# Performance work log

Hardware: AMD Instinct MI355X
Metric: run time of the kernel (lower is better)

The kernel has to match this reference:

```python
import math
import jax, jax.numpy as jnp
import numpy as np


def setup_inputs() -> dict:
    key = jax.random.key(0)
    k1, k2 = jax.random.split(key)
    N, H, W, h, d = 32, 32, 32, 16, 64
    input_NHWhd = jax.random.normal(k1, (N, H, W, h, d), dtype=jnp.float32)
    emb_2dd = jax.random.uniform(k2, (2, d, d), dtype=jnp.float32) * (2.0 * math.pi)
    return {"input_NHWhd": input_NHWhd, "emb_2dd": emb_2dd}


def _positions(H, W):
    # xlim = sqrt(W/H), ylim = sqrt(H/W); positions stacked as (y, x)
    xlim = math.sqrt(W / H)
    ylim = math.sqrt(H / W)
    x_HW = jnp.broadcast_to(jnp.linspace(-xlim, xlim, W, dtype=jnp.float32)[None, :], (H, W))
    y_HW = jnp.broadcast_to(jnp.linspace(-ylim, ylim, H, dtype=jnp.float32)[:, None], (H, W))
    return jnp.stack((y_HW, x_HW), axis=-1)  # [H, W, 2]


def reference(input_NHWhd, emb_2dd):
    N, H, W, h, d = input_NHWhd.shape
    # skew-symmetric generator bases (the -0.5 shift cancels in M - M^T,
    # kept for faithfulness to the original)
    upper_2dd = jnp.triu(emb_2dd, k=1) - 0.5
    skew_2dd = upper_2dd - jnp.swapaxes(upper_2dd, -2, -1)  # [2, d, d]
    pos_HW2 = _positions(H, W)
    # per-position generator: sum over the 2 spatial components
    gen_HWdd = jnp.einsum("hwc,cij->hwij", pos_HW2, skew_2dd)  # [H, W, d, d]
    rot_HWdd = jax.vmap(jax.scipy.linalg.expm)(gen_HWdd.reshape(-1, d, d)).reshape(H, W, d, d)
    # apply rotation: out[n,y,x,q,:] = input[n,y,x,q,:] @ rot[y,x]
    out_NHWhd = jnp.einsum("nhwqd,hwde->nhwqe", input_NHWhd, rot_HWdd.astype(input_NHWhd.dtype))
    return out_NHWhd
```

## Files before the change

### kernel.cpp

```cpp
#include <hip/hip_runtime.h>


typedef float f4 __attribute__((ext_vector_type(4)));
typedef short s8v __attribute__((ext_vector_type(8)));
typedef float f32x4 __attribute__((ext_vector_type(4)));
typedef unsigned short ush;
typedef unsigned int u32;
typedef ush us4 __attribute__((ext_vector_type(4)));

constexpr int LST = 68;
constexpr int BST = 72;
constexpr int SLOT = 64 * BST;

static __device__ __forceinline__ ush f2bf(float f) {
    u32 u = __float_as_uint(f);
    u += 0x7fffu + ((u >> 16) & 1u);
    return (ush)(u >> 16);
}
static __device__ __forceinline__ float bf2f(ush h) {
    return __uint_as_float(((u32)h) << 16);
}
static __device__ __forceinline__ s8v negbf(s8v v) {
    u32* p = (u32*)&v;
#pragma unroll
    for (int i = 0; i < 4; ++i) p[i] ^= 0x80008000u;
    return v;
}
static __device__ __forceinline__ u32 cvtpk(float a, float b) {
    u32 r;
    asm("v_cvt_pk_bf16_f32 %0, %1, %2" : "=v"(r) : "v"(a), "v"(b));
    return r;
}

static __device__ __forceinline__ void load_frag(
    s8v fr[2][2][2], const ush* __restrict__ ah, const ush* __restrict__ al,
    int m, int q4, int base, bool neg)
{
#pragma unroll
    for (int t = 0; t < 2; ++t)
#pragma unroll
        for (int ks = 0; ks < 2; ++ks) {
            const int off = (base + t * 16 + m) * BST + ks * 32 + q4 * 8;
            s8v h = *(const s8v*)&ah[off];
            s8v l = *(const s8v*)&al[off];
            if (neg) { h = negbf(h); l = negbf(l); }
            fr[t][ks][0] = h;
            fr[t][ks][1] = l;
        }
}

static __device__ __forceinline__ void mm_pre(
    ush* __restrict__ dh, ush* __restrict__ dl,
    const s8v pa[2][2][2],
    const ush* __restrict__ qh, const ush* __restrict__ ql,
    float cdiag, int m, int q4, int DM, int DN)
{
    s8v qb[2][2][2];
    load_frag(qb, qh, ql, m, q4, DN, false);

    f32x4 acc[2][2];
#pragma unroll
    for (int mt = 0; mt < 2; ++mt)
#pragma unroll
        for (int nt = 0; nt < 2; ++nt) acc[mt][nt] = (f32x4){0.f, 0.f, 0.f, 0.f};

#pragma unroll
    for (int ks = 0; ks < 2; ++ks)
#pragma unroll
        for (int mt = 0; mt < 2; ++mt)
#pragma unroll
            for (int nt = 0; nt < 2; ++nt) {
                acc[mt][nt] = __builtin_amdgcn_mfma_f32_16x16x32_bf16(
                    pa[mt][ks][0], qb[nt][ks][0], acc[mt][nt], 0, 0, 0);
                acc[mt][nt] = __builtin_amdgcn_mfma_f32_16x16x32_bf16(
                    pa[mt][ks][0], qb[nt][ks][1], acc[mt][nt], 0, 0, 0);
                acc[mt][nt] = __builtin_amdgcn_mfma_f32_16x16x32_bf16(
                    pa[mt][ks][1], qb[nt][ks][0], acc[mt][nt], 0, 0, 0);
            }

#pragma unroll
    for (int mt = 0; mt < 2; ++mt)
#pragma unroll
        for (int nt = 0; nt < 2; ++nt) {
            const int gm = DM + mt * 16 + q4 * 4;
            const int gn = DN + nt * 16 + m;
            us4 h4, l4;
#pragma unroll
            for (int r = 0; r < 4; ++r) {
                float v = acc[mt][nt][r];
                if (gn == gm + r) v += cdiag;
                const ush h = f2bf(v);
                h4[r] = h;
                l4[r] = f2bf(v - bf2f(h));
            }
            *(us4*)&dh[gn * BST + gm] = h4;
            *(us4*)&dl[gn * BST + gm] = l4;
        }
}

static __device__ __forceinline__ void transp(
    ush* __restrict__ dh, ush* __restrict__ dl,
    const ush* __restrict__ sh, const ush* __restrict__ sl, int tid)
{
    const int r = tid & 63;
    const int k0 = (tid >> 6) << 4;
    s8v a0 = *(const s8v*)&sh[r * BST + k0];
    s8v a1 = *(const s8v*)&sh[r * BST + k0 + 8];
    s8v b0 = *(const s8v*)&sl[r * BST + k0];
    s8v b1 = *(const s8v*)&sl[r * BST + k0 + 8];
#pragma unroll
    for (int j = 0; j < 8; ++j) {
        dh[(k0 + j) * BST + r]     = ((const ush*)&a0)[j];
        dh[(k0 + j + 8) * BST + r] = ((const ush*)&a1)[j];
        dl[(k0 + j) * BST + r]     = ((const ush*)&b0)[j];
        dl[(k0 + j + 8) * BST + r] = ((const ush*)&b1)[j];
    }
}

__global__ __launch_bounds__(256, 2)
void liere_expm(const float* __restrict__ emb, ush* __restrict__ ws) {
    __shared__ __align__(16) ush buf[6 * SLOT];
    __shared__ float snorm;

    const int tid = threadIdx.x;
    const int p = blockIdx.x;
    const int y = p >> 5;
    const int x = p & 31;

    float* sG = (float*)(buf);
    float* sU = (float*)(buf + 2 * SLOT);
    float* sV = (float*)(buf + 4 * SLOT);

#pragma unroll
    for (int i = 0; i < 4; ++i) {
        int lin = i * 1024 + tid * 4;
        int r = lin >> 6, c = lin & 63;
        *(f4*)&sU[r * LST + c] = *(const f4*)&emb[lin];
        *(f4*)&sV[r * LST + c] = *(const f4*)&emb[4096 + lin];
    }
    __syncthreads();

    const float yv = (2.0f * (float)y - 31.0f) / 31.0f;
    const float xv = (2.0f * (float)x - 31.0f) / 31.0f;
    {
        const int r0 = (tid >> 4) << 2, c0 = (tid & 15) << 2;
#pragma unroll
        for (int i = 0; i < 4; ++i)
#pragma unroll
            for (int j = 0; j < 4; ++j) {
                int r = r0 + i, c = c0 + j;
                float s0, s1;
                if (r < c)      { s0 = sU[r * LST + c];  s1 = sV[r * LST + c]; }
                else if (r > c) { s0 = -sU[c * LST + r]; s1 = -sV[c * LST + r]; }
                else            { s0 = 0.f; s1 = 0.f; }
                sG[r * LST + c] = yv * s0 + xv * s1;
            }
    }
    __syncthreads();

    if (tid < 64) {
        float s = 0.f;
        for (int c = 0; c < 64; ++c) s += fabsf(sG[tid * LST + c]);
#pragma unroll
        for (int off = 32; off > 0; off >>= 1) s = fmaxf(s, __shfl_down(s, off, 64));
        if (tid == 0) snorm = s;
    }
    __syncthreads();
    int sq = 0;
    {
        float nm = snorm;
        if (nm > 1.0f) sq = (int)ceilf(log2f(nm));
        if (sq < 0) sq = 0;
        if (sq > 14) sq = 14;
    }
    const float scale = exp2f((float)(-sq));

    const float C9 = 2.75573192e-6f, C8 = 2.48015876e-5f, C7 = 1.98412701e-4f,
                C6 = 1.38888893e-3f, C5 = 8.33333377e-3f, C4 = 4.16666679e-2f,
                C3 = 0.166666672f,   C2 = 0.5f,           C1 = 1.0f, C0 = 1.0f;

    ush* Xh = buf + 2 * SLOT;  ush* Xl = buf + 3 * SLOT;
    ush* t_h = buf + 4 * SLOT; ush* t_l = buf + 5 * SLOT;
    ush* u_h = buf + 0 * SLOT; ush* u_l = buf + 1 * SLOT;

    {
        const int r0 = (tid >> 4) << 2, c0 = (tid & 15) << 2;
#pragma unroll
        for (int i = 0; i < 4; ++i)
#pragma unroll
            for (int j = 0; j < 4; ++j) {
                int r = r0 + i, c = c0 + j;
                float a = sG[r * LST + c] * scale;
                ush xh = f2bf(a);
                Xh[r * BST + c] = xh;
                Xl[r * BST + c] = f2bf(a - bf2f(xh));
                float t0 = C9 * a + ((r == c) ? C8 : 0.f);
                ush th = f2bf(t0);
                t_h[r * BST + c] = th;
                t_l[r * BST + c] = f2bf(t0 - bf2f(th));
            }
    }
    __syncthreads();

    const int lane = tid & 63;
    const int w = tid >> 6;
    const int m = lane & 15;
    const int q4 = lane >> 4;
    const int DM = (w & 1) * 32;
    const int DN = (w >> 1) * 32;

    s8v xf[2][2][2];
    load_frag(xf, Xh, Xl, m, q4, DM, true);

    const float cs[8] = {C7, C6, C5, C4, C3, C2, C1, C0};
#pragma unroll
    for (int s = 0; s < 8; ++s) {
        mm_pre(u_h, u_l, xf, t_h, t_l, cs[s], m, q4, DM, DN);
        __syncthreads();
        ush* th2 = t_h; t_h = u_h; u_h = th2;
        ush* tl2 = t_l; t_l = u_l; u_l = tl2;
    }
    ush* tt_h = Xh; ush* tt_l = Xl;
    transp(tt_h, tt_l, t_h, t_l, tid);
    __syncthreads();

    for (int i = 0; i < sq; ++i) {
        s8v af[2][2][2];
        load_frag(af, tt_h, tt_l, m, q4, DM, false);
        mm_pre(u_h, u_l, af, t_h, t_l, 0.f, m, q4, DM, DN);
        __syncthreads();
        transp(tt_h, tt_l, u_h, u_l, tid);
        __syncthreads();
        ush* th2 = t_h; t_h = u_h; u_h = th2;
        ush* tl2 = t_l; t_l = u_l; u_l = tl2;
    }
    {
        const int pos0 = y * 32 + x;
        const int pos1 = (31 - y) * 32 + (31 - x);
        ush* A0 = ws + (size_t)pos0 * 4096;
        ush* A1 = ws + (size_t)pos1 * 4096;
        const int r = tid >> 2;
        const int c = (tid & 3) << 4;
        s8v v0 = *(const s8v*)&tt_h[r * BST + c];
        s8v v1 = *(const s8v*)&tt_h[r * BST + c + 8];
        s8v w0 = *(const s8v*)&t_h[r * BST + c];
        s8v w1 = *(const s8v*)&t_h[r * BST + c + 8];
        *(s8v*)&A0[r * 64 + c] = v0;
        *(s8v*)&A0[r * 64 + c + 8] = v1;
        *(s8v*)&A1[r * 64 + c] = w0;
        *(s8v*)&A1[r * 64 + c + 8] = w1;
    }
}

__global__ __launch_bounds__(256, 5)
void liere_apply(const float* __restrict__ in, const ush* __restrict__ ws,
                 float* __restrict__ out) {
    const int tid = threadIdx.x;
    const int b = blockIdx.x;
    const int posid = b >> 1;
    const int half = b & 1;
    const int w = tid >> 6;
    const int lane = tid & 63;
    const int m = lane & 15;
    const int q4 = lane >> 4;

    const ush* RF = ws + (size_t)posid * 4096;
    s8v rf[4][2];
#pragma unroll
    for (int t = 0; t < 4; ++t) {
        rf[t][0] = *(const s8v*)&RF[(t * 16 + m) * 64 + q4 * 8];
        rf[t][1] = *(const s8v*)&RF[(t * 16 + m) * 64 + 32 + q4 * 8];
    }

    const size_t pos = (size_t)posid * 1024;
    const int n0 = half * 16 + w * 4;

    for (int i = 0; i < 4; ++i) {
        const int n = n0 + i;
        const size_t nb = (size_t)n << 20;
        const float* src = in + nb + pos + m * 64 + q4 * 8;
        f4 u0 = *(const f4*)src;
        f4 u1 = *(const f4*)(src + 4);
        f4 u2 = *(const f4*)(src + 32);
        f4 u3 = *(const f4*)(src + 36);

        union { s8v v; u32 wv[4]; } B0, B1;
        B0.wv[0] = cvtpk(u0.x, u0.y); B0.wv[1] = cvtpk(u0.z, u0.w);
        B0.wv[2] = cvtpk(u1.x, u1.y); B0.wv[3] = cvtpk(u1.z, u1.w);
        B1.wv[0] = cvtpk(u2.x, u2.y); B1.wv[1] = cvtpk(u2.z, u2.w);
        B1.wv[2] = cvtpk(u3.x, u3.y); B1.wv[3] = cvtpk(u3.z, u3.w);

        f32x4 acc0 = {0.f,0.f,0.f,0.f}, acc1 = acc0, acc2 = acc0, acc3 = acc0;
        acc0 = __builtin_amdgcn_mfma_f32_16x16x32_bf16(rf[0][0], B0.v, acc0, 0, 0, 0);
        acc0 = __builtin_amdgcn_mfma_f32_16x16x32_bf16(rf[0][1], B1.v, acc0, 0, 0, 0);
        acc1 = __builtin_amdgcn_mfma_f32_16x16x32_bf16(rf[1][0], B0.v, acc1, 0, 0, 0);
        acc1 = __builtin_amdgcn_mfma_f32_16x16x32_bf16(rf[1][1], B1.v, acc1, 0, 0, 0);
        acc2 = __builtin_amdgcn_mfma_f32_16x16x32_bf16(rf[2][0], B0.v, acc2, 0, 0, 0);
        acc2 = __builtin_amdgcn_mfma_f32_16x16x32_bf16(rf[2][1], B1.v, acc2, 0, 0, 0);
        acc3 = __builtin_amdgcn_mfma_f32_16x16x32_bf16(rf[3][0], B0.v, acc3, 0, 0, 0);
        acc3 = __builtin_amdgcn_mfma_f32_16x16x32_bf16(rf[3][1], B1.v, acc3, 0, 0, 0);

        float* dst = out + nb + pos + m * 64 + q4 * 4;
        f4 o0 = {acc0[0], acc0[1], acc0[2], acc0[3]};
        f4 o1 = {acc1[0], acc1[1], acc1[2], acc1[3]};
        f4 o2 = {acc2[0], acc2[1], acc2[2], acc2[3]};
        f4 o3 = {acc3[0], acc3[1], acc3[2], acc3[3]};
        *(f4*)(dst +  0) = o0;
        *(f4*)(dst + 16) = o1;
        *(f4*)(dst + 32) = o2;
        *(f4*)(dst + 48) = o3;
    }
}

__global__ __launch_bounds__(256, 2)
void liere_fused(const float* __restrict__ in, const float* __restrict__ emb,
                 float* __restrict__ out) {
    __shared__ __align__(16) ush buf[6 * SLOT];
    __shared__ float snorm;

    const int tid = threadIdx.x;
    const int p = blockIdx.x;
    const int y = p >> 5;
    const int x = p & 31;

    float* sG = (float*)(buf);
    float* sU = (float*)(buf + 2 * SLOT);
    float* sV = (float*)(buf + 4 * SLOT);

#pragma unroll
    for (int i = 0; i < 4; ++i) {
        int lin = i * 1024 + tid * 4;
        int r = lin >> 6, c = lin & 63;
        *(f4*)&sU[r * LST + c] = *(const f4*)&emb[lin];
        *(f4*)&sV[r * LST + c] = *(const f4*)&emb[4096 + lin];
    }
    __syncthreads();

    const float yv = (2.0f * (float)y - 31.0f) / 31.0f;
    const float xv = (2.0f * (float)x - 31.0f) / 31.0f;
    {
        const int r0 = (tid >> 4) << 2, c0 = (tid & 15) << 2;
#pragma unroll
        for (int i = 0; i < 4; ++i)
#pragma unroll
            for (int j = 0; j < 4; ++j) {
                int r = r0 + i, c = c0 + j;
                float s0, s1;
                if (r < c)      { s0 = sU[r * LST + c];  s1 = sV[r * LST + c]; }
                else if (r > c) { s0 = -sU[c * LST + r]; s1 = -sV[c * LST + r]; }
                else            { s0 = 0.f; s1 = 0.f; }
                sG[r * LST + c] = yv * s0 + xv * s1;
            }
    }
    __syncthreads();

    if (tid < 64) {
        float s = 0.f;
        for (int c = 0; c < 64; ++c) s += fabsf(sG[tid * LST + c]);
#pragma unroll
        for (int off = 32; off > 0; off >>= 1) s = fmaxf(s, __shfl_down(s, off, 64));
        if (tid == 0) snorm = s;
    }
    __syncthreads();
    int sq = 0;
    {
        float nm = snorm;
        if (nm > 1.0f) sq = (int)ceilf(log2f(nm));
        if (sq < 0) sq = 0;
        if (sq > 14) sq = 14;
    }
    const float scale = exp2f((float)(-sq));

    const float C9 = 2.75573192e-6f, C8 = 2.48015876e-5f, C7 = 1.98412701e-4f,
                C6 = 1.38888893e-3f, C5 = 8.33333377e-3f, C4 = 4.16666679e-2f,
                C3 = 0.166666672f,   C2 = 0.5f,           C1 = 1.0f, C0 = 1.0f;

    ush* Xh = buf + 2 * SLOT;  ush* Xl = buf + 3 * SLOT;
    ush* t_h = buf + 4 * SLOT; ush* t_l = buf + 5 * SLOT;
    ush* u_h = buf + 0 * SLOT; ush* u_l = buf + 1 * SLOT;

    {
        const int r0 = (tid >> 4) << 2, c0 = (tid & 15) << 2;
#pragma unroll
        for (int i = 0; i < 4; ++i)
#pragma unroll
            for (int j = 0; j < 4; ++j) {
                int r = r0 + i, c = c0 + j;
                float a = sG[r * LST + c] * scale;
                ush xh = f2bf(a);
                Xh[r * BST + c] = xh;
                Xl[r * BST + c] = f2bf(a - bf2f(xh));
                float t0 = C9 * a + ((r == c) ? C8 : 0.f);
                ush th = f2bf(t0);
                t_h[r * BST + c] = th;
                t_l[r * BST + c] = f2bf(t0 - bf2f(th));
            }
    }
    __syncthreads();

    const int lane = tid & 63;
    const int w = tid >> 6;
    const int m = lane & 15;
    const int q4 = lane >> 4;
    const int DM = (w & 1) * 32;
    const int DN = (w >> 1) * 32;

    s8v xf[2][2][2];
    load_frag(xf, Xh, Xl, m, q4, DM, true);

    const float cs[8] = {C7, C6, C5, C4, C3, C2, C1, C0};
#pragma unroll
    for (int s = 0; s < 8; ++s) {
        mm_pre(u_h, u_l, xf, t_h, t_l, cs[s], m, q4, DM, DN);
        __syncthreads();
        ush* th2 = t_h; t_h = u_h; u_h = th2;
        ush* tl2 = t_l; t_l = u_l; u_l = tl2;
    }
    ush* tt_h = Xh; ush* tt_l = Xl;
    transp(tt_h, tt_l, t_h, t_l, tid);
    __syncthreads();

    for (int i = 0; i < sq; ++i) {
        s8v af[2][2][2];
        load_frag(af, tt_h, tt_l, m, q4, DM, false);
        mm_pre(u_h, u_l, af, t_h, t_l, 0.f, m, q4, DM, DN);
        __syncthreads();
        transp(tt_h, tt_l, u_h, u_l, tid);
        __syncthreads();
        ush* th2 = t_h; t_h = u_h; u_h = th2;
        ush* tl2 = t_l; t_l = u_l; u_l = tl2;
    }

    const int pass = w >> 1;
    const int nbase = (w & 1) << 4;

    const ush* RF = pass ? t_h : tt_h;
    s8v rf[4][2];
#pragma unroll
    for (int t = 0; t < 4; ++t) {
        rf[t][0] = *(const s8v*)&RF[(t * 16 + m) * BST + q4 * 8];
        rf[t][1] = *(const s8v*)&RF[(t * 16 + m) * BST + 32 + q4 * 8];
    }

    const int yy = pass ? (31 - y) : y;
    const int xx = pass ? (31 - x) : x;
    const size_t pos = (size_t)(yy * 32 + xx) * 1024;

    for (int i = 0; i < 16; ++i) {
        const int n = nbase + i;
        const size_t nb = (size_t)n << 20;
        const float* src = in + nb + pos + m * 64 + q4 * 8;
        f4 u0 = *(const f4*)src;
        f4 u1 = *(const f4*)(src + 4);
        f4 u2 = *(const f4*)(src + 32);
        f4 u3 = *(const f4*)(src + 36);
        union { s8v v; u32 wv[4]; } B0, B1;
        B0.wv[0] = cvtpk(u0.x, u0.y); B0.wv[1] = cvtpk(u0.z, u0.w);
        B0.wv[2] = cvtpk(u1.x, u1.y); B0.wv[3] = cvtpk(u1.z, u1.w);
        B1.wv[0] = cvtpk(u2.x, u2.y); B1.wv[1] = cvtpk(u2.z, u2.w);
        B1.wv[2] = cvtpk(u3.x, u3.y); B1.wv[3] = cvtpk(u3.z, u3.w);

        f32x4 acc0 = {0.f,0.f,0.f,0.f}, acc1 = acc0, acc2 = acc0, acc3 = acc0;
        acc0 = __builtin_amdgcn_mfma_f32_16x16x32_bf16(rf[0][0], B0.v, acc0, 0, 0, 0);
        acc0 = __builtin_amdgcn_mfma_f32_16x16x32_bf16(rf[0][1], B1.v, acc0, 0, 0, 0);
        acc1 = __builtin_amdgcn_mfma_f32_16x16x32_bf16(rf[1][0], B0.v, acc1, 0, 0, 0);
        acc1 = __builtin_amdgcn_mfma_f32_16x16x32_bf16(rf[1][1], B1.v, acc1, 0, 0, 0);
        acc2 = __builtin_amdgcn_mfma_f32_16x16x32_bf16(rf[2][0], B0.v, acc2, 0, 0, 0);
        acc2 = __builtin_amdgcn_mfma_f32_16x16x32_bf16(rf[2][1], B1.v, acc2, 0, 0, 0);
        acc3 = __builtin_amdgcn_mfma_f32_16x16x32_bf16(rf[3][0], B0.v, acc3, 0, 0, 0);
        acc3 = __builtin_amdgcn_mfma_f32_16x16x32_bf16(rf[3][1], B1.v, acc3, 0, 0, 0);

        float* dst = out + nb + pos + m * 64 + q4 * 4;
        f4 o0 = {acc0[0], acc0[1], acc0[2], acc0[3]};
        f4 o1 = {acc1[0], acc1[1], acc1[2], acc1[3]};
        f4 o2 = {acc2[0], acc2[1], acc2[2], acc2[3]};
        f4 o3 = {acc3[0], acc3[1], acc3[2], acc3[3]};
        *(f4*)(dst +  0) = o0;
        *(f4*)(dst + 16) = o1;
        *(f4*)(dst + 32) = o2;
        *(f4*)(dst + 48) = o3;
    }
}

extern "C" void kernel_launch(void* const* d_in, const int* in_sizes, int n_in,
                              void* d_out, int out_size, void* d_ws, size_t ws_size,
                              hipStream_t stream) {
    (void)in_sizes; (void)n_in; (void)out_size;
    const float* in = (const float*)d_in[0];
    const float* emb = (const float*)d_in[1];
    float* out = (float*)d_out;
    const size_t need = (size_t)1024 * 4096 * sizeof(ush);
    if (d_ws != nullptr && ws_size >= need) {
        ush* ws = (ush*)d_ws;
        hipLaunchKernelGGL(liere_expm, dim3(512), dim3(256), 0, stream, emb, ws);
        hipLaunchKernelGGL(liere_apply, dim3(2048), dim3(256), 0, stream, in, ws, out);
    } else {
        hipLaunchKernelGGL(liere_fused, dim3(512), dim3(256), 0, stream, in, emb, out);
    }
}
```

Before: 287.2 us.

## Prefetch input tiles two iterations ahead and use one block per position

The apply kernel now runs one block per spatial position with each wave handling 8 batch items, so each block loads its rotation fragments once instead of twice. It software-pipelines the global loads with a 3-slot register ring, prefetching two iterations ahead, and writes the output with nontemporal stores. The intent is to hide memory latency and cut duplicated rotation-matrix loads in this bandwidth-bound kernel. The cost is more registers (launch bounds lowered to 4) and half as many blocks, which reduces available parallelism.

```diff
diff --git a/kernel.cpp b/kernel.cpp
--- a/kernel.cpp
+++ b/kernel.cpp
@@ -252,13 +252,11 @@
     }
 }
 
-__global__ __launch_bounds__(256, 5)
+__global__ __launch_bounds__(256, 4)
 void liere_apply(const float* __restrict__ in, const ush* __restrict__ ws,
                  float* __restrict__ out) {
     const int tid = threadIdx.x;
-    const int b = blockIdx.x;
-    const int posid = b >> 1;
-    const int half = b & 1;
+    const int posid = blockIdx.x;
     const int w = tid >> 6;
     const int lane = tid & 63;
     const int m = lane & 15;
@@ -273,22 +271,36 @@
     }
 
     const size_t pos = (size_t)posid * 1024;
-    const int n0 = half * 16 + w * 4;
-
-    for (int i = 0; i < 4; ++i) {
-        const int n = n0 + i;
-        const size_t nb = (size_t)n << 20;
-        const float* src = in + nb + pos + m * 64 + q4 * 8;
-        f4 u0 = *(const f4*)src;
-        f4 u1 = *(const f4*)(src + 4);
-        f4 u2 = *(const f4*)(src + 32);
-        f4 u3 = *(const f4*)(src + 36);
+    const int n0 = w * 8;
+    const int moff = m * 64 + q4 * 8;
+
+    f4 u[3][4];
+
+#define LIERE_LD(slot, it) do { \
+        const size_t nb_ = (size_t)(n0 + (it)) << 20; \
+        const float* s_ = in + nb_ + pos + moff; \
+        u[slot][0] = *(const f4*)s_; \
+        u[slot][1] = *(const f4*)(s_ + 4); \
+        u[slot][2] = *(const f4*)(s_ + 32); \
+        u[slot][3] = *(const f4*)(s_ + 36); \
+    } while (0)
+
+    LIERE_LD(0, 0);
+    LIERE_LD(1, 1);
+
+#pragma unroll
+    for (int i = 0; i < 8; ++i) {
+        if (i + 2 < 8) {
+            const int ps = (i + 2) % 3;
+            LIERE_LD(ps, i + 2);
+        }
+        const int s = i % 3;
 
         union { s8v v; u32 wv[4]; } B0, B1;
-        B0.wv[0] = cvtpk(u0.x, u0.y); B0.wv[1] = cvtpk(u0.z, u0.w);
-        B0.wv[2] = cvtpk(u1.x, u1.y); B0.wv[3] = cvtpk(u1.z, u1.w);
-        B1.wv[0] = cvtpk(u2.x, u2.y); B1.wv[1] = cvtpk(u2.z, u2.w);
-        B1.wv[2] = cvtpk(u3.x, u3.y); B1.wv[3] = cvtpk(u3.z, u3.w);
+        B0.wv[0] = cvtpk(u[s][0].x, u[s][0].y); B0.wv[1] = cvtpk(u[s][0].z, u[s][0].w);
+        B0.wv[2] = cvtpk(u[s][1].x, u[s][1].y); B0.wv[3] = cvtpk(u[s][1].z, u[s][1].w);
+        B1.wv[0] = cvtpk(u[s][2].x, u[s][2].y); B1.wv[1] = cvtpk(u[s][2].z, u[s][2].w);
+        B1.wv[2] = cvtpk(u[s][3].x, u[s][3].y); B1.wv[3] = cvtpk(u[s][3].z, u[s][3].w);
 
         f32x4 acc0 = {0.f,0.f,0.f,0.f}, acc1 = acc0, acc2 = acc0, acc3 = acc0;
         acc0 = __builtin_amdgcn_mfma_f32_16x16x32_bf16(rf[0][0], B0.v, acc0, 0, 0, 0);
@@ -300,16 +312,18 @@
         acc3 = __builtin_amdgcn_mfma_f32_16x16x32_bf16(rf[3][0], B0.v, acc3, 0, 0, 0);
         acc3 = __builtin_amdgcn_mfma_f32_16x16x32_bf16(rf[3][1], B1.v, acc3, 0, 0, 0);
 
+        const size_t nb = (size_t)(n0 + i) << 20;
         float* dst = out + nb + pos + m * 64 + q4 * 4;
         f4 o0 = {acc0[0], acc0[1], acc0[2], acc0[3]};
         f4 o1 = {acc1[0], acc1[1], acc1[2], acc1[3]};
         f4 o2 = {acc2[0], acc2[1], acc2[2], acc2[3]};
         f4 o3 = {acc3[0], acc3[1], acc3[2], acc3[3]};
-        *(f4*)(dst +  0) = o0;
-        *(f4*)(dst + 16) = o1;
-        *(f4*)(dst + 32) = o2;
-        *(f4*)(dst + 48) = o3;
-    }
+        __builtin_nontemporal_store(o0, (f4*)(dst +  0));
+        __builtin_nontemporal_store(o1, (f4*)(dst + 16));
+        __builtin_nontemporal_store(o2, (f4*)(dst + 32));
+        __builtin_nontemporal_store(o3, (f4*)(dst + 48));
+    }
+#undef LIERE_LD
 }
 
 __global__ __launch_bounds__(256, 2)
@@ -493,7 +507,7 @@
     if (d_ws != nullptr && ws_size >= need) {
         ush* ws = (ush*)d_ws;
         hipLaunchKernelGGL(liere_expm, dim3(512), dim3(256), 0, stream, emb, ws);
-        hipLaunchKernelGGL(liere_apply, dim3(2048), dim3(256), 0, stream, in, ws, out);
+        hipLaunchKernelGGL(liere_apply, dim3(1024), dim3(256), 0, stream, in, ws, out);
     } else {
         hipLaunchKernelGGL(liere_fused, dim3(512), dim3(256), 0, stream, in, emb, out);
     }
```

Result: no change. 286.4 us (-0.3%).
